# Kernel tuning notes

Hardware: AMD Instinct MI355X
Metric: run time of the kernel (lower is better)

The kernel has to match this reference:

```python
import jax, jax.numpy as jnp
import numpy as np


def setup_inputs() -> dict:
    key = jax.random.key(0)
    k1, k2, k3, k4 = jax.random.split(key, 4)
    B, W, S, C, h, w = 8, 5, 5, 640, 10, 10  # episodes, n_way, n_shot, channels, feat HxW
    Q = 75  # queries per episode
    return {
        "x_shot": jax.random.normal(k1, (B, W, S, C, h, w), dtype=jnp.float32),
        "x_query": jax.random.normal(k2, (B, Q, C, h, w), dtype=jnp.float32),
        "r_cos": jax.random.normal(k3, (1,), dtype=jnp.float32),
        "r_dn4": jax.random.normal(k4, (1,), dtype=jnp.float32),
        "neighbor_k": 5,
    }


def reference(x_shot, x_query, r_cos, r_dn4, neighbor_k):
    B, W, S, C, h, w = x_shot.shape
    Q = x_query.shape[1]
    hw = h * w

    base = x_shot.reshape(B, W, S, C, hw)            # [B,W,S,C,hw]
    query = x_query.reshape(B, Q, C, hw)             # [B,Q,C,hw]

    # --- cosine prototype branch ---
    base_mean = base.mean(axis=4)                    # [B,W,S,C] GAP
    proto = base_mean.mean(axis=2)                   # [B,W,C]
    q_mean = query.mean(axis=3)                      # [B,Q,C]
    qn = q_mean / jnp.linalg.norm(q_mean, axis=-1, keepdims=True)
    pn = proto / jnp.linalg.norm(proto, axis=-1, keepdims=True)
    logits_cos = jnp.einsum('bqc,bwc->bqw', qn, pn)  # [B,Q,W]

    # --- DN4 local-descriptor branch ---
    # support descriptors: [B,W,S*hw,C]
    base_mix = jnp.transpose(base, (0, 1, 2, 4, 3)).reshape(B, W, S * hw, C)
    # NOTE: original code normalizes support along the DESCRIPTOR axis (dim 0 of [S*hw,C]),
    # i.e. per-channel across descriptors. Reproduce that faithfully.
    sup = base_mix / jnp.linalg.norm(base_mix, axis=2, keepdims=True)
    # query descriptors: [B,Q,hw,C], L2-normalized per descriptor (over C)
    qd = jnp.transpose(query, (0, 1, 3, 2))
    qd = qd / jnp.linalg.norm(qd, axis=-1, keepdims=True)

    # patch-wise similarity: [B,Q,W,hw,S*hw]
    sim = jnp.einsum('bqpc,bwdc->bqwpd', qd, sup)
    topv, _ = jax.lax.top_k(sim, neighbor_k)         # [B,Q,W,hw,k]
    # original: sum over ALL (hw rows x k) top values, divided by neighbor_k
    logits_dn4 = topv.sum(axis=(-1, -2)) / neighbor_k  # [B,Q,W]

    return r_cos * logits_cos + r_dn4 * logits_dn4
```

## Files before the change

kernel.cpp:

```cpp
#include <hip/hip_runtime.h>
#include <cstddef>

typedef unsigned short u16;
typedef _Float16 f16x8 __attribute__((ext_vector_type(8)));
typedef float f32x4 __attribute__((ext_vector_type(4)));

#define NB  8
#define NW  5
#define NS  5
#define NC  640
#define NHW 100
#define NQ  75
#define ND  500
#define NDP 512
#define NR  7500
#define NRP 7552
#define NRT 59

#define OFF_SUP   ((size_t)0)
#define OFF_ABF   ((size_t)26214400)
#define OFF_QRN   ((size_t)103546880)
#define OFF_PROTO ((size_t)103788544)

__device__ __forceinline__ u16 f2h_bits(float x) {
  _Float16 h = (_Float16)x;
  return __builtin_bit_cast(u16, h);
}
__device__ __forceinline__ float h2f_bits(u16 u) {
  return (float)__builtin_bit_cast(_Float16, u);
}

__device__ __forceinline__ float block_sum(float v, float* sc, int t) {
  v += __shfl_xor(v, 32, 64);
  v += __shfl_xor(v, 16, 64);
  v += __shfl_xor(v, 8, 64);
  v += __shfl_xor(v, 4, 64);
  v += __shfl_xor(v, 2, 64);
  v += __shfl_xor(v, 1, 64);
  __syncthreads();
  if ((t & 63) == 0) sc[t >> 6] = v;
  __syncthreads();
  return sc[0] + sc[1] + sc[2] + sc[3];
}

__device__ __forceinline__ void t5_insert(float (&t5)[5], float v) {
  if (v > t5[0]) {
    t5[0] = v; float tmp;
    if (t5[0] > t5[1]) { tmp = t5[0]; t5[0] = t5[1]; t5[1] = tmp; }
    if (t5[1] > t5[2]) { tmp = t5[1]; t5[1] = t5[2]; t5[2] = tmp; }
    if (t5[2] > t5[3]) { tmp = t5[2]; t5[2] = t5[3]; t5[3] = tmp; }
    if (t5[3] > t5[4]) { tmp = t5[3]; t5[3] = t5[4]; t5[4] = tmp; }
  }
}

__global__ __launch_bounds__(256) void k1_sup(const float* __restrict__ xs,
                                              u16* __restrict__ sup2,
                                              float* __restrict__ proto_g) {
  const int cc = blockIdx.x, w = blockIdx.y, b = blockIdx.z;
  const int t = threadIdx.x;
  __shared__ u16 tile[512 * 34];
  __shared__ float rn[32];
  const size_t bw = (size_t)b * NW + w;
  const float* xbase = xs + bw * NS * NC * NHW;
  const int cb = cc * 32;

  for (int s = 0; s < NS; s++) {
    const float4* rb = (const float4*)(xbase + ((size_t)s * NC + cb) * NHW);
    for (int i4 = t; i4 < 800; i4 += 256) {
      const float4 v = rb[i4];
      const int c = i4 / 25, p4 = i4 % 25;
      const int d = s * NHW + p4 * 4;
      tile[(d    ) * 34 + c] = f2h_bits(v.x);
      tile[(d + 1) * 34 + c] = f2h_bits(v.y);
      tile[(d + 2) * 34 + c] = f2h_bits(v.z);
      tile[(d + 3) * 34 + c] = f2h_bits(v.w);
    }
  }
  if (t < 384) tile[(500 + (t >> 5)) * 34 + (t & 31)] = 0;
  __syncthreads();
  {
    const int c = t >> 3, part = t & 7;
    float ss = 0.f, sm = 0.f;
    for (int d = part; d < ND; d += 8) {
      const float x = h2f_bits(tile[d * 34 + c]);
      ss += x * x; sm += x;
    }
    ss += __shfl_xor(ss, 1, 64); ss += __shfl_xor(ss, 2, 64); ss += __shfl_xor(ss, 4, 64);
    sm += __shfl_xor(sm, 1, 64); sm += __shfl_xor(sm, 2, 64); sm += __shfl_xor(sm, 4, 64);
    if (part == 0) {
      rn[c] = 1.0f / sqrtf(ss);
      proto_g[bw * NC + cb + c] = sm;
    }
  }
  __syncthreads();
  u16* obase = sup2 + bw * NDP * NC + cb;
  for (int idx = t; idx < 512 * 32; idx += 256) {
    const int cl = idx & 31, d = idx >> 5;
    obase[(size_t)d * NC + cl] = f2h_bits(h2f_bits(tile[d * 34 + cl]) * rn[cl]);
  }
}

__global__ __launch_bounds__(256) void k2_query(const float* __restrict__ xq,
                                                const float* __restrict__ proto_g,
                                                const float* __restrict__ rcosp,
                                                u16* __restrict__ Abf,
                                                float* __restrict__ qrn,
                                                float* __restrict__ out) {
  const int q = blockIdx.x, b = blockIdx.y;
  const int t = threadIdx.x;
  __shared__ u16 tile[128 * 106];
  __shared__ float qm[NC];
  __shared__ float qs[NHW];
  __shared__ float sc[4];
  const float* xbase = xq + ((size_t)b * NQ + q) * NC * NHW;
  u16* abase = Abf + ((size_t)b * NRP + (size_t)q * NHW) * NC;

  if (t < NHW) qs[t] = 0.f;
  __syncthreads();

  for (int cc = 0; cc < 5; cc++) {
    const float4* rb = (const float4*)(xbase + (size_t)cc * 128 * NHW);
    for (int i4 = t; i4 < 3200; i4 += 256) {
      const float4 xv = rb[i4];
      const int e = i4 * 4;
      const int p = e % NHW, cl = e / NHW;
      const unsigned lo = (unsigned)f2h_bits(xv.x) | ((unsigned)f2h_bits(xv.y) << 16);
      const unsigned hi = (unsigned)f2h_bits(xv.z) | ((unsigned)f2h_bits(xv.w) << 16);
      unsigned* tw = (unsigned*)&tile[cl * 106 + p];
      tw[0] = lo; tw[1] = hi;
    }
    __syncthreads();
    if (t < 128) {
      float s = 0.f;
      const unsigned* row = (const unsigned*)&tile[t * 106];
      for (int j = 0; j < 50; j++) {
        const unsigned u = row[j];
        s += h2f_bits((u16)(u & 0xffffu)) + h2f_bits((u16)(u >> 16));
      }
      qm[cc * 128 + t] = s;
    } else if (t < 228) {
      const int p = t - 128;
      float s = 0.f;
      for (int c = 0; c < 128; c++) {
        const float x = h2f_bits(tile[c * 106 + p]);
        s += x * x;
      }
      qs[p] += s;
    }
    {
      const int c0 = t & 63, pr = t >> 6;
      for (int p = pr; p < NHW; p += 4) {
        abase[(size_t)p * NC + cc * 128 + c0]      = tile[c0 * 106 + p];
        abase[(size_t)p * NC + cc * 128 + c0 + 64] = tile[(c0 + 64) * 106 + p];
      }
    }
    __syncthreads();
  }
  if (t < NHW) qrn[(size_t)b * NRP + q * NHW + t] = 1.0f / sqrtf(qs[t]);

  float part = 0.f;
  for (int c = t; c < NC; c += 256) part += qm[c] * qm[c];
  const float qq = block_sum(part, sc, t);
  const float rcos = rcosp[0];
  for (int w = 0; w < NW; w++) {
    const float* pr_ = proto_g + ((size_t)b * NW + w) * NC;
    float dp = 0.f, pp = 0.f;
    for (int c = t; c < NC; c += 256) { const float pv = pr_[c]; dp += qm[c] * pv; pp += pv * pv; }
    dp = block_sum(dp, sc, t);
    pp = block_sum(pp, sc, t);
    if (t == 0) out[((size_t)b * NQ + q) * NW + w] = rcos * dp / sqrtf(qq * pp);
  }
  if (q == 0) {
    u16* pz = Abf + ((size_t)b * NRP + NR) * NC;
    for (int i = t; i < (NRP - NR) * NC; i += 256) pz[i] = 0;
  }
}

__global__ __launch_bounds__(256, 3) void k4_dn4(const u16* __restrict__ Abf,
                                                 const u16* __restrict__ sup2,
                                                 const float* __restrict__ qrn,
                                                 const float* __restrict__ rdn4p,
                                                 const int* __restrict__ nkp,
                                                 float* __restrict__ out) {
  const int rt = blockIdx.x, w = blockIdx.y, b = blockIdx.z;
  const int t = threadIdx.x;
  const int lane = t & 63, wid = t >> 6;
  const int m = lane & 15, quad = lane >> 4;
  const int wx = wid & 1, wy = wid >> 1;

  __shared__ __align__(16) u16 stg[2][2][128 * 40];

  const u16* Ab = Abf + ((size_t)b * NRP + (size_t)rt * 128) * NC;
  const u16* Bb = sup2 + ((size_t)b * NW + w) * NDP * NC;

  const int rr = t >> 2;
  const int c8 = (t & 3) * 8;

  uint4 ra0, ra1, rb0, rb1;

#define G_LOAD2(CT_, K0_) do {                                            \
    const u16* ap_ = Ab + (size_t)rr * NC + (K0_) + c8;                   \
    ra0 = *(const uint4*)ap_;                                             \
    ra1 = *(const uint4*)(ap_ + (size_t)64 * NC);                         \
    const u16* bp_ = Bb + (size_t)((CT_) * 128 + rr) * NC + (K0_) + c8;   \
    rb0 = *(const uint4*)bp_;                                             \
    rb1 = *(const uint4*)(bp_ + (size_t)64 * NC);                         \
  } while (0)

#define LDS_STORE(BUF_) do {                                              \
    *(uint4*)&stg[BUF_][0][rr * 40 + c8]        = ra0;                    \
    *(uint4*)&stg[BUF_][0][(rr + 64) * 40 + c8] = ra1;                    \
    *(uint4*)&stg[BUF_][1][rr * 40 + c8]        = rb0;                    \
    *(uint4*)&stg[BUF_][1][(rr + 64) * 40 + c8] = rb1;                    \
  } while (0)

  float t5[4][5];
#pragma unroll
  for (int qt = 0; qt < 4; qt++)
#pragma unroll
    for (int i = 0; i < 5; i++) t5[qt][i] = -3e38f;

  G_LOAD2(0, 0);
  LDS_STORE(0);
  G_LOAD2(0, 32);
  __syncthreads();

  for (int ct = 0; ct < 4; ct++) {
    f32x4 acc[4][4];
#pragma unroll
    for (int dt = 0; dt < 4; dt++)
#pragma unroll
      for (int qt = 0; qt < 4; qt++)
        acc[dt][qt] = (f32x4){0.f, 0.f, 0.f, 0.f};

    for (int s = 0; s < 20; s++) {
      if (!(ct == 3 && s == 19)) LDS_STORE((s + 1) & 1);
      if (!(ct == 3 && s >= 18)) {
        const int ctn = (s < 18) ? ct : ct + 1;
        const int k0n = ((s < 18) ? (s + 2) : (s - 18)) * 32;
        G_LOAD2(ctn, k0n);
      }
      {
        const u16* la = &stg[s & 1][0][0];
        const u16* lb = &stg[s & 1][1][0];
        f16x8 af0, af1, af2, af3, bf0, bf1, bf2, bf3;
        af0 = *(const f16x8*)&la[(wy * 64 +  0 + m) * 40 + quad * 8];
        af1 = *(const f16x8*)&la[(wy * 64 + 16 + m) * 40 + quad * 8];
        af2 = *(const f16x8*)&la[(wy * 64 + 32 + m) * 40 + quad * 8];
        af3 = *(const f16x8*)&la[(wy * 64 + 48 + m) * 40 + quad * 8];
        bf0 = *(const f16x8*)&lb[(wx * 64 +  0 + m) * 40 + quad * 8];
        bf1 = *(const f16x8*)&lb[(wx * 64 + 16 + m) * 40 + quad * 8];
        bf2 = *(const f16x8*)&lb[(wx * 64 + 32 + m) * 40 + quad * 8];
        bf3 = *(const f16x8*)&lb[(wx * 64 + 48 + m) * 40 + quad * 8];
        acc[0][0] = __builtin_amdgcn_mfma_f32_16x16x32_f16(bf0, af0, acc[0][0], 0, 0, 0);
        acc[0][1] = __builtin_amdgcn_mfma_f32_16x16x32_f16(bf0, af1, acc[0][1], 0, 0, 0);
        acc[0][2] = __builtin_amdgcn_mfma_f32_16x16x32_f16(bf0, af2, acc[0][2], 0, 0, 0);
        acc[0][3] = __builtin_amdgcn_mfma_f32_16x16x32_f16(bf0, af3, acc[0][3], 0, 0, 0);
        acc[1][0] = __builtin_amdgcn_mfma_f32_16x16x32_f16(bf1, af0, acc[1][0], 0, 0, 0);
        acc[1][1] = __builtin_amdgcn_mfma_f32_16x16x32_f16(bf1, af1, acc[1][1], 0, 0, 0);
        acc[1][2] = __builtin_amdgcn_mfma_f32_16x16x32_f16(bf1, af2, acc[1][2], 0, 0, 0);
        acc[1][3] = __builtin_amdgcn_mfma_f32_16x16x32_f16(bf1, af3, acc[1][3], 0, 0, 0);
        acc[2][0] = __builtin_amdgcn_mfma_f32_16x16x32_f16(bf2, af0, acc[2][0], 0, 0, 0);
        acc[2][1] = __builtin_amdgcn_mfma_f32_16x16x32_f16(bf2, af1, acc[2][1], 0, 0, 0);
        acc[2][2] = __builtin_amdgcn_mfma_f32_16x16x32_f16(bf2, af2, acc[2][2], 0, 0, 0);
        acc[2][3] = __builtin_amdgcn_mfma_f32_16x16x32_f16(bf2, af3, acc[2][3], 0, 0, 0);
        acc[3][0] = __builtin_amdgcn_mfma_f32_16x16x32_f16(bf3, af0, acc[3][0], 0, 0, 0);
        acc[3][1] = __builtin_amdgcn_mfma_f32_16x16x32_f16(bf3, af1, acc[3][1], 0, 0, 0);
        acc[3][2] = __builtin_amdgcn_mfma_f32_16x16x32_f16(bf3, af2, acc[3][2], 0, 0, 0);
        acc[3][3] = __builtin_amdgcn_mfma_f32_16x16x32_f16(bf3, af3, acc[3][3], 0, 0, 0);
      }
      __syncthreads();
    }

    const int dlim = ND - ct * 128 - wx * 64;
    if (dlim >= 64) {
#pragma unroll
      for (int dt = 0; dt < 4; dt++)
#pragma unroll
        for (int qt = 0; qt < 4; qt++)
#pragma unroll
          for (int r = 0; r < 4; r++)
            t5_insert(t5[qt], acc[dt][qt][r]);
    } else {
#pragma unroll
      for (int dt = 0; dt < 4; dt++)
#pragma unroll
        for (int qt = 0; qt < 4; qt++)
#pragma unroll
          for (int r = 0; r < 4; r++)
            if (dt * 16 + quad * 4 + r < dlim) t5_insert(t5[qt], acc[dt][qt][r]);
    }
  }

#pragma unroll
  for (int qt = 0; qt < 4; qt++) {
    float rec[5];
#pragma unroll
    for (int i = 0; i < 5; i++) rec[i] = __shfl_xor(t5[qt][i], 16, 64);
#pragma unroll
    for (int i = 0; i < 5; i++) t5_insert(t5[qt], rec[i]);
#pragma unroll
    for (int i = 0; i < 5; i++) rec[i] = __shfl_xor(t5[qt][i], 32, 64);
#pragma unroll
    for (int i = 0; i < 5; i++) t5_insert(t5[qt], rec[i]);
  }

  float* scratch = (float*)&stg[0][0][0];
  if (wx == 1 && quad == 0) {
#pragma unroll
    for (int qt = 0; qt < 4; qt++) {
      const int row = wy * 64 + qt * 16 + m;
#pragma unroll
      for (int i = 0; i < 5; i++) scratch[row * 5 + i] = t5[qt][i];
    }
  }
  __syncthreads();
  if (wx == 0 && quad == 0) {
    const float scale = rdn4p[0] / (float)nkp[0];
#pragma unroll
    for (int qt = 0; qt < 4; qt++) {
      const int row = wy * 64 + qt * 16 + m;
#pragma unroll
      for (int i = 0; i < 5; i++) t5_insert(t5[qt], scratch[row * 5 + i]);
      const int r = rt * 128 + row;
      if (r < NR) {
        const float s = t5[qt][0] + t5[qt][1] + t5[qt][2] + t5[qt][3] + t5[qt][4];
        const float contrib = s * qrn[(size_t)b * NRP + r] * scale;
        const int qi = r / NHW;
        atomicAdd(&out[((size_t)b * NQ + qi) * NW + w], contrib);
      }
    }
  }
#undef G_LOAD2
#undef LDS_STORE
}

extern "C" void kernel_launch(void* const* d_in, const int* in_sizes, int n_in,
                              void* d_out, int out_size, void* d_ws, size_t ws_size,
                              hipStream_t stream) {
  (void)in_sizes; (void)n_in; (void)out_size; (void)ws_size;
  const float* xs   = (const float*)d_in[0];
  const float* xq   = (const float*)d_in[1];
  const float* rcos = (const float*)d_in[2];
  const float* rdn4 = (const float*)d_in[3];
  const int*   nk   = (const int*)d_in[4];
  float* out = (float*)d_out;
  char* ws = (char*)d_ws;
  u16*   sup2  = (u16*)(ws + OFF_SUP);
  u16*   Abf   = (u16*)(ws + OFF_ABF);
  float* qrn   = (float*)(ws + OFF_QRN);
  float* proto = (float*)(ws + OFF_PROTO);

  k1_sup <<<dim3(20, NW, NB),  dim3(256), 0, stream>>>(xs, sup2, proto);
  k2_query<<<dim3(NQ, NB),     dim3(256), 0, stream>>>(xq, proto, rcos, Abf, qrn, out);
  k4_dn4 <<<dim3(NRT, NW, NB), dim3(256), 0, stream>>>(Abf, sup2, qrn, rdn4, nk, out);
}
```

Baseline: 508.7 us.

## Store LDS tiles in MFMA fragment order and swizzle blocks across XCDs

Replaces the padded row-major LDS staging with a layout where each lane's 8-element fragment is contiguous, so both LDS stores and MFMA operand loads are linear and avoid bank conflicts. Global loads are remapped so each thread fetches the rows it will store in this order. The 3D grid is flattened and remapped so blocks placed on the same XCD share episode and row-tile, aiming at better L2 reuse of the query and support tiles. Also reduces LDS footprint, at the cost of less coalesced global access patterns and extra index arithmetic.

```diff
diff --git a/kernel.cpp b/kernel.cpp
--- a/kernel.cpp
+++ b/kernel.cpp
@@ -182,36 +182,47 @@
                                                  const float* __restrict__ rdn4p,
                                                  const int* __restrict__ nkp,
                                                  float* __restrict__ out) {
-  const int rt = blockIdx.x, w = blockIdx.y, b = blockIdx.z;
+  const int id = blockIdx.x;
+  const int j = (id & 7) * 295 + (id >> 3);
+  const int w = j % 5;
+  const int v = j / 5;
+  const int rt = v % NRT;
+  const int b = v / NRT;
+
   const int t = threadIdx.x;
   const int lane = t & 63, wid = t >> 6;
   const int m = lane & 15, quad = lane >> 4;
   const int wx = wid & 1, wy = wid >> 1;
 
-  __shared__ __align__(16) u16 stg[2][2][128 * 40];
+  __shared__ __align__(16) u16 stg[2][2][4096];
 
   const u16* Ab = Abf + ((size_t)b * NRP + (size_t)rt * 128) * NC;
   const u16* Bb = sup2 + ((size_t)b * NW + w) * NDP * NC;
 
-  const int rr = t >> 2;
-  const int c8 = (t & 3) * 8;
+  const int row0 = ((t >> 6) << 4) | (t & 15);
+  const int qc = (t >> 4) & 3;
+  const size_t aoff = (size_t)row0 * NC + qc * 8;
+  const size_t a64 = (size_t)64 * NC;
+  const int tt8 = t * 8;
+  const int lane8 = lane * 8;
+  const int wyo = wy * 2048, wxo = wx * 2048;
 
   uint4 ra0, ra1, rb0, rb1;
 
 #define G_LOAD2(CT_, K0_) do {                                            \
-    const u16* ap_ = Ab + (size_t)rr * NC + (K0_) + c8;                   \
+    const u16* ap_ = Ab + aoff + (K0_);                                   \
     ra0 = *(const uint4*)ap_;                                             \
-    ra1 = *(const uint4*)(ap_ + (size_t)64 * NC);                         \
-    const u16* bp_ = Bb + (size_t)((CT_) * 128 + rr) * NC + (K0_) + c8;   \
+    ra1 = *(const uint4*)(ap_ + a64);                                     \
+    const u16* bp_ = Bb + (size_t)(CT_) * (128 * NC) + aoff + (K0_);      \
     rb0 = *(const uint4*)bp_;                                             \
-    rb1 = *(const uint4*)(bp_ + (size_t)64 * NC);                         \
+    rb1 = *(const uint4*)(bp_ + a64);                                     \
   } while (0)
 
 #define LDS_STORE(BUF_) do {                                              \
-    *(uint4*)&stg[BUF_][0][rr * 40 + c8]        = ra0;                    \
-    *(uint4*)&stg[BUF_][0][(rr + 64) * 40 + c8] = ra1;                    \
-    *(uint4*)&stg[BUF_][1][rr * 40 + c8]        = rb0;                    \
-    *(uint4*)&stg[BUF_][1][(rr + 64) * 40 + c8] = rb1;                    \
+    *(uint4*)&stg[BUF_][0][tt8]        = ra0;                             \
+    *(uint4*)&stg[BUF_][0][tt8 + 2048] = ra1;                             \
+    *(uint4*)&stg[BUF_][1][tt8]        = rb0;                             \
+    *(uint4*)&stg[BUF_][1][tt8 + 2048] = rb1;                             \
   } while (0)
 
   float t5[4][5];
@@ -241,17 +252,17 @@
         G_LOAD2(ctn, k0n);
       }
       {
-        const u16* la = &stg[s & 1][0][0];
-        const u16* lb = &stg[s & 1][1][0];
+        const u16* la_ = &stg[s & 1][0][wyo];
+        const u16* lb_ = &stg[s & 1][1][wxo];
         f16x8 af0, af1, af2, af3, bf0, bf1, bf2, bf3;
-        af0 = *(const f16x8*)&la[(wy * 64 +  0 + m) * 40 + quad * 8];
-        af1 = *(const f16x8*)&la[(wy * 64 + 16 + m) * 40 + quad * 8];
-        af2 = *(const f16x8*)&la[(wy * 64 + 32 + m) * 40 + quad * 8];
-        af3 = *(const f16x8*)&la[(wy * 64 + 48 + m) * 40 + quad * 8];
-        bf0 = *(const f16x8*)&lb[(wx * 64 +  0 + m) * 40 + quad * 8];
-        bf1 = *(const f16x8*)&lb[(wx * 64 + 16 + m) * 40 + quad * 8];
-        bf2 = *(const f16x8*)&lb[(wx * 64 + 32 + m) * 40 + quad * 8];
-        bf3 = *(const f16x8*)&lb[(wx * 64 + 48 + m) * 40 + quad * 8];
+        af0 = *(const f16x8*)&la_[lane8];
+        af1 = *(const f16x8*)&la_[lane8 + 512];
+        af2 = *(const f16x8*)&la_[lane8 + 1024];
+        af3 = *(const f16x8*)&la_[lane8 + 1536];
+        bf0 = *(const f16x8*)&lb_[lane8];
+        bf1 = *(const f16x8*)&lb_[lane8 + 512];
+        bf2 = *(const f16x8*)&lb_[lane8 + 1024];
+        bf3 = *(const f16x8*)&lb_[lane8 + 1536];
         acc[0][0] = __builtin_amdgcn_mfma_f32_16x16x32_f16(bf0, af0, acc[0][0], 0, 0, 0);
         acc[0][1] = __builtin_amdgcn_mfma_f32_16x16x32_f16(bf0, af1, acc[0][1], 0, 0, 0);
         acc[0][2] = __builtin_amdgcn_mfma_f32_16x16x32_f16(bf0, af2, acc[0][2], 0, 0, 0);
@@ -291,6 +302,8 @@
             if (dt * 16 + quad * 4 + r < dlim) t5_insert(t5[qt], acc[dt][qt][r]);
     }
   }
+#undef G_LOAD2
+#undef LDS_STORE
 
 #pragma unroll
   for (int qt = 0; qt < 4; qt++) {
@@ -317,6 +330,7 @@
   __syncthreads();
   if (wx == 0 && quad == 0) {
     const float scale = rdn4p[0] / (float)nkp[0];
+    const float* qrb = qrn + (size_t)b * NRP;
 #pragma unroll
     for (int qt = 0; qt < 4; qt++) {
       const int row = wy * 64 + qt * 16 + m;
@@ -325,14 +339,12 @@
       const int r = rt * 128 + row;
       if (r < NR) {
         const float s = t5[qt][0] + t5[qt][1] + t5[qt][2] + t5[qt][3] + t5[qt][4];
-        const float contrib = s * qrn[(size_t)b * NRP + r] * scale;
+        const float contrib = s * qrb[r] * scale;
         const int qi = r / NHW;
         atomicAdd(&out[((size_t)b * NQ + qi) * NW + w], contrib);
       }
     }
   }
-#undef G_LOAD2
-#undef LDS_STORE
 }
 
 extern "C" void kernel_launch(void* const* d_in, const int* in_sizes, int n_in,
@@ -353,5 +365,5 @@
 
   k1_sup <<<dim3(20, NW, NB),  dim3(256), 0, stream>>>(xs, sup2, proto);
   k2_query<<<dim3(NQ, NB),     dim3(256), 0, stream>>>(xq, proto, rcos, Abf, qrn, out);
-  k4_dn4 <<<dim3(NRT, NW, NB), dim3(256), 0, stream>>>(Abf, sup2, qrn, rdn4, nk, out);
-}
+  k4_dn4 <<<dim3(NRT * NW * NB), dim3(256), 0, stream>>>(Abf, sup2, qrn, rdn4, nk, out);
+}
```

New measurement: 793.7 us. 1.56x slower.
